# Performance work log

Measured on AMD Instinct MI355X. Metric: run time of the kernel, lower is better.

The kernel has to match this reference:

```python
import jax, jax.numpy as jnp
import numpy as np

D_MODEL = 512
H = 8
D_K = D_MODEL // H


def setup_inputs() -> dict:
    key = jax.random.key(0)
    ks = jax.random.split(key, 11)
    B, S = 2, 2048
    scale = 1.0 / np.sqrt(D_MODEL)
    return {
        "q": jax.random.normal(ks[0], (B, S, D_MODEL), jnp.float32),
        "v": jax.random.normal(ks[1], (B, S, D_MODEL), jnp.float32),
        "k": jax.random.normal(ks[2], (B, S, D_MODEL), jnp.float32),
        "w_q": jax.random.normal(ks[3], (D_MODEL, D_MODEL), jnp.float32) * scale,
        "b_q": jnp.zeros((D_MODEL,), jnp.float32),
        "w_k": jax.random.normal(ks[4], (D_MODEL, D_MODEL), jnp.float32) * scale,
        "b_k": jnp.zeros((D_MODEL,), jnp.float32),
        "w_v": jax.random.normal(ks[5], (D_MODEL, D_MODEL), jnp.float32) * scale,
        "b_v": jnp.zeros((D_MODEL,), jnp.float32),
        "w_o": jax.random.normal(ks[6], (D_MODEL, D_MODEL), jnp.float32) * scale,
        "b_o": jnp.zeros((D_MODEL,), jnp.float32),
    }


def reference(q, v, k, w_q, b_q, w_k, b_k, w_v, b_v, w_o, b_o):
    B, S, _ = q.shape
    # projections (nn.Linear: x @ W.T + b)
    query = q @ w_q.T + b_q
    key_t = k @ w_k.T + b_k
    value = v @ w_v.T + b_v
    # split heads: [B, S, H, D_K] -> [B, H, S, D_K]
    query = query.reshape(B, S, H, D_K).transpose(0, 2, 1, 3)
    key_t = key_t.reshape(B, S, H, D_K).transpose(0, 2, 1, 3)
    value = value.reshape(B, S, H, D_K).transpose(0, 2, 1, 3)
    # unfused attention: full [B, H, S, S] score matrix
    scores = jnp.einsum("bhqd,bhkd->bhqk", query, key_t) / jnp.sqrt(
        jnp.asarray(D_K, query.dtype)
    )
    attn = jax.nn.softmax(scores, axis=-1)  # dropout inactive in eval
    x = jnp.einsum("bhqk,bhkd->bhqd", attn, value)
    # merge heads and output projection
    x = x.transpose(0, 2, 1, 3).reshape(B, S, D_MODEL)
    return x @ w_o.T + b_o
```

## Files before the change

kernel.cpp:

```cpp
#include <hip/hip_runtime.h>
#include <hip/hip_bf16.h>


typedef __attribute__((ext_vector_type(8))) short short8;
typedef __attribute__((ext_vector_type(4))) short short4v;
typedef __attribute__((ext_vector_type(4))) float f32x4;
typedef __attribute__((ext_vector_type(2))) unsigned int uint2v;

#define DM 512
#define SEQ 2048
#define NROW 4096
#define LOG2E 1.44269504088896341f
#define MFMA(a, b, c) __builtin_amdgcn_mfma_f32_16x16x32_bf16(a, b, c, 0, 0, 0)
#define FENCE() __asm__ __volatile__("" ::: "memory")

#if __has_builtin(__builtin_amdgcn_exp2f)
#define EXP2(x) __builtin_amdgcn_exp2f(x)
#else
#define EXP2(x) exp2f(x)
#endif

__device__ __forceinline__ float bf_bits2f(short s) {
    unsigned int u = ((unsigned int)(unsigned short)s) << 16;
    return __builtin_bit_cast(float, u);
}
__device__ __forceinline__ short f2bf_r(float f) {
    unsigned int u = __builtin_bit_cast(unsigned int, f) + 0x8000u;
    return (short)(u >> 16);
}
__device__ __forceinline__ unsigned int pack_bf16(float lo, float hi) {
    unsigned int ul = __builtin_bit_cast(unsigned int, lo) + 0x8000u;
    unsigned int uh = __builtin_bit_cast(unsigned int, hi) + 0x8000u;
    return __builtin_amdgcn_perm(uh, ul, 0x07060302u);
}

__device__ __forceinline__ void gload_lds16(const void* src, void* lds_dst) {
    __builtin_amdgcn_global_load_lds(
        (const __attribute__((address_space(1))) unsigned int*)src,
        (__attribute__((address_space(3))) unsigned int*)lds_dst, 16, 0, 0);
}

template <int ROWS, int NW, int SH = 0>
__device__ __forceinline__ void stage_tile(const short* __restrict__ gsrc, size_t gstride,
                                           short* lds, int wave, int lane) {
    constexpr int ISSUES = ROWS * 8 / (64 * NW);
    #pragma unroll
    for (int i = 0; i < ISSUES; i++) {
        const int blk = i * NW + wave;
        const int g = blk * 64 + lane;
        const int row = g >> 3;
        const int cb = (g & 7) ^ ((row >> SH) & 7);
        gload_lds16(gsrc + (size_t)row * gstride + cb * 8, lds + (size_t)blk * 512);
    }
}

__device__ __forceinline__ bool detect_f32(const unsigned int* __restrict__ q, int* cnt_lds) {
    if (threadIdx.x == 0) *cnt_lds = 0;
    __syncthreads();
    int local = 0;
    for (int i = threadIdx.x; i < 1024; i += blockDim.x) {
        unsigned int lo = q[i] & 0x7FFFu;
        if (lo >= 0x3000u && lo < 0x4400u) local++;
    }
    if (local) atomicAdd(cnt_lds, local);
    __syncthreads();
    return *cnt_lds < 512;
}

struct ConvArgs { const void* src[11]; short* dst[11]; int n[11]; int* flag; };
__global__ void convert_all(ConvArgs a) {
    __shared__ int cnt;
    const bool f32m = detect_f32((const unsigned int*)a.src[0], &cnt);
    if (threadIdx.x == 0) *a.flag = f32m ? 1 : 0;
    const int tid = blockIdx.x * 256 + threadIdx.x;
    const int stride = gridDim.x * 256;
    if (f32m) {
        for (int s = 0; s < 11; s++) {
            const float4* sp = (const float4*)a.src[s];
            short4v* dp = (short4v*)a.dst[s];
            const int n4 = a.n[s] >> 2;
            for (int i = tid; i < n4; i += stride) {
                float4 v = sp[i];
                short4v o;
                o[0] = f2bf_r(v.x); o[1] = f2bf_r(v.y);
                o[2] = f2bf_r(v.z); o[3] = f2bf_r(v.w);
                dp[i] = o;
            }
        }
    } else {
        for (int s = 0; s < 11; s++) {
            const short4v* sp = (const short4v*)a.src[s];
            short4v* dp = (short4v*)a.dst[s];
            const int n4 = a.n[s] >> 2;
            for (int i = tid; i < n4; i += stride) dp[i] = sp[i];
        }
    }
}

template <int MT, int NT>
__device__ __forceinline__ void gemm_core(const short* __restrict__ A,
                                          const short* __restrict__ W,
                                          int m0, int n0, short* Alds, short* Blds,
                                          int wave, int lane,
                                          f32x4 (&acc)[MT / 64][NT / 16]) {
    const int rc = lane & 15, quad = lane >> 4;
    const short* Ag = A + (size_t)m0 * DM;
    const short* Bg = W + (size_t)n0 * DM;
    constexpr int ABUF = MT * 64, BBUF = NT * 64;
    constexpr int INFLIGHT = (MT + NT) * 8 / 256;
    constexpr int NITER = DM / 64;

    stage_tile<MT, 4>(Ag, DM, Alds, wave, lane);
    stage_tile<NT, 4>(Bg, DM, Blds, wave, lane);

    for (int i = 0; i < NITER; i++) {
        const int cur = i & 1;
        const short* Ac = Alds + cur * ABUF;
        const short* Bc = Blds + cur * BBUF;
        if (i + 1 < NITER) {
            stage_tile<MT, 4>(Ag + (i + 1) * 64, DM, Alds + (cur ^ 1) * ABUF, wave, lane);
            stage_tile<NT, 4>(Bg + (i + 1) * 64, DM, Blds + (cur ^ 1) * BBUF, wave, lane);
            __builtin_amdgcn_s_waitcnt(0x3F70 | INFLIGHT);
        } else {
            __builtin_amdgcn_s_waitcnt(0x3F70);
        }
        FENCE();
        __builtin_amdgcn_s_barrier();
        FENCE();
        #pragma unroll
        for (int h = 0; h < 2; h++) {
            short8 bf[NT / 16];
            #pragma unroll
            for (int nt = 0; nt < NT / 16; nt++) {
                const int br = nt * 16 + rc;
                bf[nt] = *(const short8*)&Bc[br * 64 + (((quad + 4 * h) ^ (br & 7)) * 8)];
            }
            #pragma unroll
            for (int ms = 0; ms < MT / 64; ms++) {
                const int ar = wave * (MT / 4) + ms * 16 + rc;
                short8 af = *(const short8*)&Ac[ar * 64 + (((quad + 4 * h) ^ (ar & 7)) * 8)];
                #pragma unroll
                for (int nt = 0; nt < NT / 16; nt++)
                    acc[ms][nt] = MFMA(af, bf[nt], acc[ms][nt]);
            }
        }
        FENCE();
        __builtin_amdgcn_s_barrier();
        FENCE();
    }
}

struct QKVArgs {
    const short* A[3]; const short* W[3]; const short* Bi[3];
    short* Cq; short* Ck; short* Cv;
};
__global__ __launch_bounds__(256, 2) void qkv_gemm(QKVArgs args) {
    __shared__ __align__(16) short Alds[2][128 * 64];
    __shared__ __align__(16) short Blds[2][128 * 64];
    const int z = blockIdx.z;
    const int wave = threadIdx.x >> 6, lane = threadIdx.x & 63;
    const int rc = lane & 15, quad = lane >> 4;
    const int m0 = blockIdx.x * 128, n0 = blockIdx.y * 128;

    f32x4 acc[2][8] = {};
    gemm_core<128, 128>(args.A[z], args.W[z], m0, n0, &Alds[0][0], &Blds[0][0], wave, lane, acc);
    const short* bias = args.Bi[z];

    if (z == 2) {
        #pragma unroll
        for (int ms = 0; ms < 2; ms++) {
            const int mw = m0 + wave * 32 + ms * 16;
            const int b = mw >> 11, sb = (mw & 2047) + quad * 4;
            #pragma unroll
            for (int nt = 0; nt < 8; nt++) {
                const int dg = n0 + nt * 16 + rc;
                const int hh = dg >> 6, dd = dg & 63;
                const float bv = bf_bits2f(bias[dg]);
                short4v pk;
                #pragma unroll
                for (int r = 0; r < 4; r++) pk[r] = f2bf_r(acc[ms][nt][r] + bv);
                *(short4v*)(args.Cv + ((size_t)((b * 8 + hh) * 64 + dd)) * SEQ + sb) = pk;
            }
        }
    } else {
        short* C = (z == 0) ? args.Cq : args.Ck;
        const float sc = (z == 0) ? (0.125f * LOG2E) : 1.0f;
        #pragma unroll
        for (int ms = 0; ms < 2; ms++) {
            const int mw = m0 + wave * 32 + ms * 16;
            #pragma unroll
            for (int nt = 0; nt < 8; nt++) {
                const int col = n0 + nt * 16 + rc;
                const float bv = bf_bits2f(bias[col]);
                #pragma unroll
                for (int r = 0; r < 4; r++)
                    C[(size_t)(mw + quad * 4 + r) * DM + col] = f2bf_r((acc[ms][nt][r] + bv) * sc);
            }
        }
    }
}

__global__ __launch_bounds__(256, 4) void out_gemm(
    const short* __restrict__ A, const short* __restrict__ W,
    const short* __restrict__ bias, void* __restrict__ Cout,
    const int* __restrict__ dtf) {
    __shared__ __align__(16) short Alds[2][64 * 64];
    __shared__ __align__(16) short Blds[2][64 * 64];
    const bool f32out = (*dtf != 0);
    const int wave = threadIdx.x >> 6, lane = threadIdx.x & 63;
    const int rc = lane & 15, quad = lane >> 4;
    const int m0 = blockIdx.x * 64, n0 = blockIdx.y * 64;
    f32x4 acc[1][4] = {};
    gemm_core<64, 64>(A, W, m0, n0, &Alds[0][0], &Blds[0][0], wave, lane, acc);
    const int mw = m0 + wave * 16;
    #pragma unroll
    for (int nt = 0; nt < 4; nt++) {
        const int col = n0 + nt * 16 + rc;
        const float bv = bf_bits2f(bias[col]);
        #pragma unroll
        for (int r = 0; r < 4; r++) {
            const size_t idx = (size_t)(mw + quad * 4 + r) * DM + col;
            const float val = acc[0][nt][r] + bv;
            if (f32out) ((float*)Cout)[idx] = val;
            else        ((short*)Cout)[idx] = f2bf_r(val);
        }
    }
}

__global__ __launch_bounds__(256, 2) void attn_kernel(
    const short* __restrict__ Q, const short* __restrict__ K,
    const short* __restrict__ Vt, short* __restrict__ X)
{
    __shared__ __align__(16) short Klds[2][128 * 64];
    __shared__ __align__(16) short Vlds[2][2][64 * 64];
    __shared__ __align__(16) short Plds[4][32 * 64];

    const int wave = threadIdx.x >> 6, lane = threadIdx.x & 63;
    const int rc = lane & 15, quad = lane >> 4;
    const int qh = wave & 1, kh = wave >> 1;
    const int L = blockIdx.x;
    const int bh = (L & 7) * 2 + ((L >> 3) >> 5);
    const int qb = (L >> 3) & 31;
    const size_t baseQK = (size_t)(bh >> 3) * SEQ * DM + (size_t)(bh & 7) * 64;
    const short* Qb = Q + baseQK;
    const short* Kb = K + baseQK;
    const short* Vb = Vt + (size_t)bh * 64 * SEQ;
    const int q0 = qb * 64 + qh * 32;

    short8 qa[2][2];
    #pragma unroll
    for (int ms = 0; ms < 2; ms++)
        #pragma unroll
        for (int h = 0; h < 2; h++)
            qa[ms][h] = *(const short8*)(Qb + (size_t)(q0 + ms * 16 + rc) * DM + h * 32 + quad * 8);

    short8 ones;
    #pragma unroll
    for (int j = 0; j < 8; j++) ones[j] = (short)0x3F80;

    f32x4 o[4][2] = {};
    f32x4 lsum[2] = {};
    short* Pw = &Plds[wave][0];

    int koff[4][2], voff[4][2], poff[2][2];
    #pragma unroll
    for (int kt = 0; kt < 4; kt++) {
        const int row = kh * 64 + rc * 4 + kt;
        #pragma unroll
        for (int h = 0; h < 2; h++)
            koff[kt][h] = row * 64 + (((quad + 4 * h) ^ ((row >> 2) & 7)) * 8);
    }
    #pragma unroll
    for (int dt = 0; dt < 4; dt++) {
        const int row = dt * 16 + rc;
        #pragma unroll
        for (int h = 0; h < 2; h++)
            voff[dt][h] = row * 64 + (((quad + 4 * h) ^ (row & 7)) * 8);
    }
    #pragma unroll
    for (int ms = 0; ms < 2; ms++)
        #pragma unroll
        for (int h = 0; h < 2; h++)
            poff[ms][h] = (ms * 16 + rc) * 64 + ((h * 32 + quad * 8) ^ ((rc & 7) << 3));

    stage_tile<128, 4, 2>(Kb, DM, &Klds[0][0], wave, lane);
    stage_tile<64, 4>(Vb, SEQ, &Vlds[0][0][0], wave, lane);
    stage_tile<64, 4>(Vb + 64, SEQ, &Vlds[0][1][0], wave, lane);
    __syncthreads();

    for (int it = 0; it < 16; ++it) {
        const int cur = it & 1;
        if (it + 1 < 16) {
            const int k0n = (it + 1) * 128;
            stage_tile<128, 4, 2>(Kb + (size_t)k0n * DM, DM, &Klds[cur ^ 1][0], wave, lane);
            stage_tile<64, 4>(Vb + k0n, SEQ, &Vlds[cur ^ 1][0][0], wave, lane);
            stage_tile<64, 4>(Vb + k0n + 64, SEQ, &Vlds[cur ^ 1][1][0], wave, lane);
        }

        const short* Kt = &Klds[cur][0];
        const short* Vl = &Vlds[cur][kh][0];

        short8 kf[4][2];
        #pragma unroll
        for (int kt = 0; kt < 4; kt++)
            #pragma unroll
            for (int h = 0; h < 2; h++)
                kf[kt][h] = *(const short8*)&Kt[koff[kt][h]];
        f32x4 s[2][4];
        __builtin_amdgcn_s_setprio(1);
        #pragma unroll
        for (int ms = 0; ms < 2; ms++)
            #pragma unroll
            for (int kt = 0; kt < 4; kt++) {
                f32x4 t = {};
                t = MFMA(qa[ms][0], kf[kt][0], t);
                t = MFMA(qa[ms][1], kf[kt][1], t);
                s[ms][kt] = t;
            }
        __builtin_amdgcn_s_setprio(0);
        #pragma unroll
        for (int ms = 0; ms < 2; ms++)
            #pragma unroll
            for (int r = 0; r < 4; r++) {
                const int row = ms * 16 + quad * 4 + r;
                uint2v pk;
                pk[0] = pack_bf16(EXP2(s[ms][0][r]), EXP2(s[ms][1][r]));
                pk[1] = pack_bf16(EXP2(s[ms][2][r]), EXP2(s[ms][3][r]));
                *(uint2v*)(&Pw[row * 64 + ((rc * 4) ^ ((row & 7) << 3))]) = pk;
            }
        __builtin_amdgcn_s_waitcnt(0xC07F);
        __builtin_amdgcn_sched_barrier(0);
        short8 pa[2][2];
        #pragma unroll
        for (int ms = 0; ms < 2; ms++)
            #pragma unroll
            for (int h = 0; h < 2; h++)
                pa[ms][h] = *(const short8*)(&Pw[poff[ms][h]]);
        __builtin_amdgcn_s_setprio(1);
        #pragma unroll
        for (int ms = 0; ms < 2; ms++) {
            lsum[ms] = MFMA(ones, pa[ms][0], lsum[ms]);
            lsum[ms] = MFMA(ones, pa[ms][1], lsum[ms]);
        }
        #pragma unroll
        for (int dt = 0; dt < 4; dt++) {
            short8 v0 = *(const short8*)&Vl[voff[dt][0]];
            short8 v1 = *(const short8*)&Vl[voff[dt][1]];
            #pragma unroll
            for (int ms = 0; ms < 2; ms++) {
                o[dt][ms] = MFMA(v0, pa[ms][0], o[dt][ms]);
                o[dt][ms] = MFMA(v1, pa[ms][1], o[dt][ms]);
            }
        }
        __builtin_amdgcn_s_setprio(0);
        __syncthreads();
    }

    float* OM = (float*)&Plds[0][0];
    float* LM = (float*)&Klds[0][0];
    if (kh == 1) {
        #pragma unroll
        for (int dt = 0; dt < 4; dt++)
            #pragma unroll
            for (int ms = 0; ms < 2; ms++)
                *(f32x4*)&OM[(((dt * 2 + ms) * 2 + qh) * 64 + lane) * 4] = o[dt][ms];
        #pragma unroll
        for (int ms = 0; ms < 2; ms++)
            LM[(qh * 2 + ms) * 64 + lane] = lsum[ms][0];
    }
    __syncthreads();
    if (kh == 0) {
        short* Xr = X + baseQK;
        #pragma unroll
        for (int ms = 0; ms < 2; ms++) {
            const float inv = 1.0f / (lsum[ms][0] + LM[(qh * 2 + ms) * 64 + lane]);
            const size_t rowoff = (size_t)(q0 + ms * 16 + rc) * DM;
            #pragma unroll
            for (int dt = 0; dt < 4; dt++) {
                const f32x4 op = *(const f32x4*)&OM[(((dt * 2 + ms) * 2 + qh) * 64 + lane) * 4];
                short4v pk;
                #pragma unroll
                for (int r = 0; r < 4; r++) pk[r] = f2bf_r((o[dt][ms][r] + op[r]) * inv);
                *(short4v*)(Xr + rowoff + dt * 16 + quad * 4) = pk;
            }
        }
    }
}

extern "C" void kernel_launch(void* const* d_in, const int* in_sizes, int n_in,
                              void* d_out, int out_size, void* d_ws, size_t ws_size,
                              hipStream_t stream) {
    char* ws = (char*)d_ws;
    const size_t SEQB = (size_t)NROW * DM * sizeof(short);
    const size_t WB   = (size_t)DM * DM * sizeof(short);
    const size_t BB   = (size_t)DM * sizeof(short);

    size_t off = 0;
    short* qc = (short*)(ws + off); off += SEQB;
    short* vc = (short*)(ws + off); off += SEQB;
    short* kc = (short*)(ws + off); off += SEQB;
    short* wq = (short*)(ws + off); off += WB;
    short* wk = (short*)(ws + off); off += WB;
    short* wv = (short*)(ws + off); off += WB;
    short* wo = (short*)(ws + off); off += WB;
    short* bq = (short*)(ws + off); off += BB;
    short* bk = (short*)(ws + off); off += BB;
    short* bv = (short*)(ws + off); off += BB;
    short* bo = (short*)(ws + off); off += BB;
    off = (off + 255) & ~(size_t)255;
    short* Qp  = (short*)(ws + off); off += SEQB;
    short* Kp  = (short*)(ws + off); off += SEQB;
    short* Vtp = (short*)(ws + off); off += SEQB;
    short* Xp  = (short*)(ws + off); off += SEQB;
    int*   dtf = (int*)(ws + off);  off += 256;

    ConvArgs ca;
    const void* srcs[11] = {d_in[0], d_in[1], d_in[2], d_in[3], d_in[5], d_in[7],
                            d_in[9], d_in[4], d_in[6], d_in[8], d_in[10]};
    short* dsts[11] = {qc, vc, kc, wq, wk, wv, wo, bq, bk, bv, bo};
    int ns[11] = {NROW * DM, NROW * DM, NROW * DM, DM * DM, DM * DM, DM * DM,
                  DM * DM, DM, DM, DM, DM};
    for (int i = 0; i < 11; i++) { ca.src[i] = srcs[i]; ca.dst[i] = dsts[i]; ca.n[i] = ns[i]; }
    ca.flag = dtf;
    convert_all<<<1024, 256, 0, stream>>>(ca);

    QKVArgs qa;
    qa.A[0] = qc; qa.A[1] = kc; qa.A[2] = vc;
    qa.W[0] = wq; qa.W[1] = wk; qa.W[2] = wv;
    qa.Bi[0] = bq; qa.Bi[1] = bk; qa.Bi[2] = bv;
    qa.Cq = Qp; qa.Ck = Kp; qa.Cv = Vtp;
    qkv_gemm<<<dim3(NROW / 128, DM / 128, 3), 256, 0, stream>>>(qa);

    attn_kernel<<<dim3(512), 256, 0, stream>>>(Qp, Kp, Vtp, Xp);

    out_gemm<<<dim3(NROW / 64, DM / 64), 256, 0, stream>>>(
        Xp, wo, bo, d_out, dtf);
}
```

Baseline: 144.1 us.

## Keep softmax probabilities in registers by permuting K rows at projection time

```diff
diff --git a/kernel.cpp b/kernel.cpp
--- a/kernel.cpp
+++ b/kernel.cpp
@@ -5,7 +5,7 @@
 typedef __attribute__((ext_vector_type(8))) short short8;
 typedef __attribute__((ext_vector_type(4))) short short4v;
 typedef __attribute__((ext_vector_type(4))) float f32x4;
-typedef __attribute__((ext_vector_type(2))) unsigned int uint2v;
+typedef __attribute__((ext_vector_type(4))) unsigned int uint4v;
 
 #define DM 512
 #define SEQ 2048
@@ -189,12 +189,19 @@
         for (int ms = 0; ms < 2; ms++) {
             const int mw = m0 + wave * 32 + ms * 16;
             #pragma unroll
-            for (int nt = 0; nt < 8; nt++) {
-                const int col = n0 + nt * 16 + rc;
-                const float bv = bf_bits2f(bias[col]);
+            for (int r = 0; r < 4; r++) {
+                int mrow = mw + quad * 4 + r;
+                if (z == 1) {
+                    const int u = mrow & 63;
+                    mrow = (mrow & ~63) |
+                           (16 * ((u >> 3) & 3) + 4 * (u & 3) + 2 * (u >> 5) + ((u >> 2) & 1));
+                }
                 #pragma unroll
-                for (int r = 0; r < 4; r++)
-                    C[(size_t)(mw + quad * 4 + r) * DM + col] = f2bf_r((acc[ms][nt][r] + bv) * sc);
+                for (int nt = 0; nt < 8; nt++) {
+                    const int col = n0 + nt * 16 + rc;
+                    const float bv = bf_bits2f(bias[col]);
+                    C[(size_t)mrow * DM + col] = f2bf_r((acc[ms][nt][r] + bv) * sc);
+                }
             }
         }
     }
@@ -233,7 +240,6 @@
 {
     __shared__ __align__(16) short Klds[2][128 * 64];
     __shared__ __align__(16) short Vlds[2][2][64 * 64];
-    __shared__ __align__(16) short Plds[4][32 * 64];
 
     const int wave = threadIdx.x >> 6, lane = threadIdx.x & 63;
     const int rc = lane & 15, quad = lane >> 4;
@@ -260,9 +266,8 @@
 
     f32x4 o[4][2] = {};
     f32x4 lsum[2] = {};
-    short* Pw = &Plds[wave][0];
-
-    int koff[4][2], voff[4][2], poff[2][2];
+
+    int koff[4][2], voff[4][2];
     #pragma unroll
     for (int kt = 0; kt < 4; kt++) {
         const int row = kh * 64 + rc * 4 + kt;
@@ -277,11 +282,6 @@
         for (int h = 0; h < 2; h++)
             voff[dt][h] = row * 64 + (((quad + 4 * h) ^ (row & 7)) * 8);
     }
-    #pragma unroll
-    for (int ms = 0; ms < 2; ms++)
-        #pragma unroll
-        for (int h = 0; h < 2; h++)
-            poff[ms][h] = (ms * 16 + rc) * 64 + ((h * 32 + quad * 8) ^ ((rc & 7) << 3));
 
     stage_tile<128, 4, 2>(Kb, DM, &Klds[0][0], wave, lane);
     stage_tile<64, 4>(Vb, SEQ, &Vlds[0][0][0], wave, lane);
@@ -313,29 +313,23 @@
             #pragma unroll
             for (int kt = 0; kt < 4; kt++) {
                 f32x4 t = {};
-                t = MFMA(qa[ms][0], kf[kt][0], t);
-                t = MFMA(qa[ms][1], kf[kt][1], t);
+                t = MFMA(kf[kt][0], qa[ms][0], t);
+                t = MFMA(kf[kt][1], qa[ms][1], t);
                 s[ms][kt] = t;
             }
         __builtin_amdgcn_s_setprio(0);
+        short8 pa[2][2];
         #pragma unroll
         for (int ms = 0; ms < 2; ms++)
             #pragma unroll
-            for (int r = 0; r < 4; r++) {
-                const int row = ms * 16 + quad * 4 + r;
-                uint2v pk;
-                pk[0] = pack_bf16(EXP2(s[ms][0][r]), EXP2(s[ms][1][r]));
-                pk[1] = pack_bf16(EXP2(s[ms][2][r]), EXP2(s[ms][3][r]));
-                *(uint2v*)(&Pw[row * 64 + ((rc * 4) ^ ((row & 7) << 3))]) = pk;
-            }
-        __builtin_amdgcn_s_waitcnt(0xC07F);
-        __builtin_amdgcn_sched_barrier(0);
-        short8 pa[2][2];
-        #pragma unroll
-        for (int ms = 0; ms < 2; ms++)
-            #pragma unroll
-            for (int h = 0; h < 2; h++)
-                pa[ms][h] = *(const short8*)(&Pw[poff[ms][h]]);
+            for (int h = 0; h < 2; h++) {
+                uint4v w;
+                w[0] = pack_bf16(EXP2(s[ms][2 * h][0]), EXP2(s[ms][2 * h][1]));
+                w[1] = pack_bf16(EXP2(s[ms][2 * h][2]), EXP2(s[ms][2 * h][3]));
+                w[2] = pack_bf16(EXP2(s[ms][2 * h + 1][0]), EXP2(s[ms][2 * h + 1][1]));
+                w[3] = pack_bf16(EXP2(s[ms][2 * h + 1][2]), EXP2(s[ms][2 * h + 1][3]));
+                pa[ms][h] = __builtin_bit_cast(short8, w);
+            }
         __builtin_amdgcn_s_setprio(1);
         #pragma unroll
         for (int ms = 0; ms < 2; ms++) {
@@ -356,8 +350,8 @@
         __syncthreads();
     }
 
-    float* OM = (float*)&Plds[0][0];
-    float* LM = (float*)&Klds[0][0];
+    float* OM = (float*)&Klds[0][0];
+    float* LM = (float*)&Vlds[0][0][0];
     if (kh == 1) {
         #pragma unroll
         for (int dt = 0; dt < 4; dt++)
```

Measured after the change: 146.1 us. About the same (+1.3%).
